# Performance work log

Measured on AMD Instinct MI355X. Metric: run time of the kernel, lower is better.

## Reference

```python
import jax, jax.numpy as jnp
import numpy as np

# 25 anchors (YOLOv2 VOC anchors replicated at 5 scales) -> pred channels = 25*5 = 125
_BASE = np.array([[1.3221, 1.73145], [3.19275, 4.00944], [5.05587, 8.09892],
                  [9.47112, 4.84053], [11.2364, 10.0071]], dtype=np.float32)
ANCHORS = jnp.asarray(np.concatenate([_BASE * s for s in (0.5, 0.75, 1.0, 1.25, 1.5)], axis=0))  # (25, 2)
NUM_ANCHORS = 25
OBJECT_SCALE = 5.0
NO_OBJECT_SCALE = 1.0
COORD_SCALE = 1.0
SIL_THRESH = 0.6


def _bbox_iou(x1, y1, w1, h1, x2, y2, w2, h2):
    """IoU of center-format boxes (cx, cy, w, h); broadcasts."""
    mx = jnp.minimum(x1 - w1 * 0.5, x2 - w2 * 0.5)
    Mx = jnp.maximum(x1 + w1 * 0.5, x2 + w2 * 0.5)
    my = jnp.minimum(y1 - h1 * 0.5, y2 - h2 * 0.5)
    My = jnp.maximum(y1 + h1 * 0.5, y2 + h2 * 0.5)
    cw = w1 + w2 - (Mx - mx)
    ch = h1 + h2 - (My - my)
    inter = jnp.where((cw > 0) & (ch > 0), cw * ch, 0.0)
    union = w1 * h1 + w2 * h2 - inter
    return inter / union


def setup_inputs() -> dict:
    key = jax.random.key(0)
    k1, k2 = jax.random.split(key)
    B, C, H, W = 512, NUM_ANCHORS * 5, 38, 38
    pred = jax.random.normal(k1, (B, C, H, W), dtype=jnp.float32)
    target = jax.random.uniform(k2, (B, 4), dtype=jnp.float32)  # normalized gx, gy, gw, gh
    return {"pred": pred, "target": target, "train_out": 0}


def reference(pred, target, train_out):
    B = pred.shape[0]
    H = pred.shape[2]
    W = pred.shape[3]
    A = NUM_ANCHORS
    p = pred.reshape(B, A, 5, H, W)

    # activations (these carry gradient in the original)
    txy = jax.nn.sigmoid(p[:, :, :2])          # (B,A,2,H,W)
    twh = p[:, :, 2:4]                         # (B,A,2,H,W)
    pred_conf = jax.nn.sigmoid(p[:, :, 4])     # (B,A,H,W)

    grid_x = jnp.arange(W, dtype=jnp.float32)[None, None, None, :]
    grid_y = jnp.arange(H, dtype=jnp.float32)[None, None, :, None]
    aw = ANCHORS[:, 0][None, :, None, None]
    ah = ANCHORS[:, 1][None, :, None, None]

    # decoded boxes are detached in the original (clone().detach())
    bx = txy[:, :, 0] + grid_x
    by = txy[:, :, 1] + grid_y
    bw = jnp.exp(twh[:, :, 0]) * aw
    bh = jnp.exp(twh[:, :, 1]) * ah
    pred_boxes = jax.lax.stop_gradient(jnp.stack([bx, by, bw, bh], axis=2))  # (B,A,4,H,W)

    tgt = jax.lax.stop_gradient(target)
    gx = tgt[:, 0] * W
    gy = tgt[:, 1] * H
    gw = tgt[:, 2] * W
    gh = tgt[:, 3] * H

    # conf_mask: zero where any pred box overlaps gt above sil_thresh
    ious = _bbox_iou(pred_boxes[:, :, 0], pred_boxes[:, :, 1], pred_boxes[:, :, 2], pred_boxes[:, :, 3],
                     gx[:, None, None, None], gy[:, None, None, None],
                     gw[:, None, None, None], gh[:, None, None, None])  # (B,A,H,W)
    conf_mask = jnp.where(ious > SIL_THRESH, 0.0, NO_OBJECT_SCALE)

    # best anchor per gt by wh-only IoU
    a_iou = _bbox_iou(0.0, 0.0, ANCHORS[:, 0][None, :], ANCHORS[:, 1][None, :],
                      0.0, 0.0, gw[:, None], gh[:, None])  # (B,A)
    best = jnp.argmax(a_iou, axis=1)  # (B,)

    gi = gx.astype(jnp.int32)
    gj = gy.astype(jnp.int32)
    bidx = jnp.arange(B)
    best_aw = ANCHORS[best, 0]
    best_ah = ANCHORS[best, 1]

    # seen < 12800 branch: coord_mask all ones, target xy default 0.5
    coord_mask = jnp.ones((B, A, H, W), dtype=jnp.float32)
    target_box = jnp.zeros((B, A, 4, H, W), dtype=jnp.float32).at[:, :, :2].set(0.5)
    target_box = target_box.at[bidx, best, 0, gj, gi].set(gx - gi)
    target_box = target_box.at[bidx, best, 1, gj, gi].set(gy - gj)
    target_box = target_box.at[bidx, best, 2, gj, gi].set(jnp.log(gw / best_aw))
    target_box = target_box.at[bidx, best, 3, gj, gi].set(jnp.log(gh / best_ah))
    conf_mask = conf_mask.at[bidx, best, gj, gi].set(OBJECT_SCALE)

    pb = pred_boxes[bidx, best, :, gj, gi]  # (B,4) pred box at gt cell
    tconf = _bbox_iou(pb[:, 0], pb[:, 1], pb[:, 2], pb[:, 3], gx, gy, gw, gh)
    target_conf = jnp.zeros((B, A, H, W), dtype=jnp.float32).at[bidx, best, gj, gi].set(tconf)

    conf_mask = jnp.sqrt(conf_mask)

    def mse_sum(a, b):
        return jnp.sum((a - b) ** 2)

    loss_x = COORD_SCALE * mse_sum(txy[:, :, 0] * coord_mask, target_box[:, :, 0] * coord_mask) / 2.0
    loss_y = COORD_SCALE * mse_sum(txy[:, :, 1] * coord_mask, target_box[:, :, 1] * coord_mask) / 2.0
    loss_w = COORD_SCALE * mse_sum(twh[:, :, 0] * coord_mask, target_box[:, :, 2] * coord_mask) / 2.0
    loss_h = COORD_SCALE * mse_sum(twh[:, :, 1] * coord_mask, target_box[:, :, 3] * coord_mask) / 2.0
    loss_conf = mse_sum(pred_conf * conf_mask, target_conf * conf_mask) / 2.0
    loss = loss_x + loss_y + loss_w + loss_h + loss_conf

    if train_out:
        return (loss, loss_x, loss_y, loss_w, loss_h, loss_conf)
    return loss
```

## Files before the change

kernel.cpp:

```cpp
#include <hip/hip_runtime.h>
#include <math.h>

#define GW 38
#define GH 38
#define NA 25
#define NB 512
#define HW (GW * GH)
#define S4 (HW / 4)
#define PLANES (NB * NA)
#define T_TOTAL (PLANES * S4)
#define BLK 256
#define NBLOCKS (T_TOTAL / BLK)

typedef float f32x4 __attribute__((ext_vector_type(4)));

struct Meta {
    float gxlo, gxhi, gylo, gyhi;
    float gw, gh, area;
    float tconf, tb0, tb1, tb2, tb3;
    int   best, cell;
};
static_assert(sizeof(Meta) == 56, "Meta layout drifted; workspace offsets depend on it");

__device__ __forceinline__ float fast_rcp(float x) { return __builtin_amdgcn_rcpf(x); }
__device__ __forceinline__ float fast_exp(float x) { return __expf(x); }
__device__ __forceinline__ float fast_sig(float x) { return fast_rcp(1.0f + fast_exp(-x)); }

__device__ __forceinline__ float iou_precise(float x1, float y1, float w1, float h1,
                                             float x2, float y2, float w2, float h2) {
    float mx = fminf(x1 - w1 * 0.5f, x2 - w2 * 0.5f);
    float Mx = fmaxf(x1 + w1 * 0.5f, x2 + w2 * 0.5f);
    float my = fminf(y1 - h1 * 0.5f, y2 - h2 * 0.5f);
    float My = fmaxf(y1 + h1 * 0.5f, y2 + h2 * 0.5f);
    float cw = w1 + w2 - (Mx - mx);
    float ch = h1 + h2 - (My - my);
    float inter = (cw > 0.0f && ch > 0.0f) ? cw * ch : 0.0f;
    float uni = w1 * h1 + w2 * h2 - inter;
    return inter / uni;
}

__device__ __forceinline__ void anchor_wh(int a, float* aw, float* ah) {
    const float bw[5] = {1.3221f, 3.19275f, 5.05587f, 9.47112f, 11.2364f};
    const float bh[5] = {1.73145f, 4.00944f, 8.09892f, 4.84053f, 10.0071f};
    float s = 0.5f + 0.25f * (float)(a / 5);
    *aw = bw[a % 5] * s;
    *ah = bh[a % 5] * s;
}

__global__ void meta_kernel(const float* __restrict__ pred,
                            const float* __restrict__ target,
                            Meta* __restrict__ metas) {
    int b = blockIdx.x * blockDim.x + threadIdx.x;
    if (b >= NB) return;
    float gx = target[b * 4 + 0] * (float)GW;
    float gy = target[b * 4 + 1] * (float)GH;
    float gw = target[b * 4 + 2] * (float)GW;
    float gh = target[b * 4 + 3] * (float)GH;
    int best = 0;
    float best_iou = -1.0f;
    for (int a = 0; a < NA; ++a) {
        float aw, ah;
        anchor_wh(a, &aw, &ah);
        float v = iou_precise(0.0f, 0.0f, aw, ah, 0.0f, 0.0f, gw, gh);
        if (v > best_iou) { best_iou = v; best = a; }
    }
    int gi = (int)gx;
    int gj = (int)gy;
    float aw, ah;
    anchor_wh(best, &aw, &ah);
    size_t base = (size_t)b * NA * 5 * HW + (size_t)(best * 5) * HW + gj * GW + gi;
    float p0 = pred[base + 0 * HW];
    float p1 = pred[base + 1 * HW];
    float p2 = pred[base + 2 * HW];
    float p3 = pred[base + 3 * HW];
    float pbx = 1.0f / (1.0f + expf(-p0)) + (float)gi;
    float pby = 1.0f / (1.0f + expf(-p1)) + (float)gj;
    float pbw = expf(p2) * aw;
    float pbh = expf(p3) * ah;
    Meta m;
    m.gxlo = gx - gw * 0.5f; m.gxhi = gx + gw * 0.5f;
    m.gylo = gy - gh * 0.5f; m.gyhi = gy + gh * 0.5f;
    m.gw = gw; m.gh = gh; m.area = gw * gh;
    m.tconf = iou_precise(pbx, pby, pbw, pbh, gx, gy, gw, gh);
    m.tb0 = gx - (float)gi;
    m.tb1 = gy - (float)gj;
    m.tb2 = logf(gw / aw);
    m.tb3 = logf(gh / ah);
    m.best = best;
    m.cell = gj * GW + gi;
    metas[b] = m;
}

__device__ __forceinline__ float cell_loss(float p0, float p1, float p2, float p3, float p4,
                                           float fi, float fj, bool obj,
                                           const Meta& m, float aw, float ah) {
    float tx = fast_sig(p0);
    float ty = fast_sig(p1);
    float conf = fast_sig(p4);
    float bw = fast_exp(p2) * aw;
    float bh = fast_exp(p3) * ah;
    float bx = tx + fi;
    float by = ty + fj;
    float mx = fminf(bx - bw * 0.5f, m.gxlo);
    float Mx = fmaxf(bx + bw * 0.5f, m.gxhi);
    float my = fminf(by - bh * 0.5f, m.gylo);
    float My = fmaxf(by + bh * 0.5f, m.gyhi);
    float cw = bw + m.gw - (Mx - mx);
    float ch = bh + m.gh - (My - my);
    float inter = (cw > 0.0f && ch > 0.0f) ? cw * ch : 0.0f;
    float uni = bw * bh + m.area - inter;
    float iou = inter * fast_rcp(uni);
    float cm = obj ? 2.23606797749979f : ((iou > 0.6f) ? 0.0f : 1.0f);
    float dx = tx - (obj ? m.tb0 : 0.5f);
    float dy = ty - (obj ? m.tb1 : 0.5f);
    float dw = p2 - (obj ? m.tb2 : 0.0f);
    float dh = p3 - (obj ? m.tb3 : 0.0f);
    float dc = cm * (conf - (obj ? m.tconf : 0.0f));
    return dx * dx + dy * dy + dw * dw + dh * dh + dc * dc;
}

template <bool USE_PARTIALS>
__global__ __launch_bounds__(BLK) void loss_kernel(const float* __restrict__ pred,
                                                   const Meta* __restrict__ metas,
                                                   float* __restrict__ sink) {
    unsigned t = blockIdx.x * (unsigned)BLK + threadIdx.x;
    unsigned plane = t / (unsigned)S4;
    unsigned s4 = t - plane * (unsigned)S4;
    unsigned b = plane / (unsigned)NA;
    unsigned a = plane - b * (unsigned)NA;

    const f32x4* base = (const f32x4*)(pred + (size_t)plane * 5u * (unsigned)HW);

    f32x4 q[5];
#pragma unroll
    for (int c = 0; c < 5; ++c)
        q[c] = __builtin_nontemporal_load(base + s4 + (unsigned)c * (unsigned)S4);

    Meta m = metas[b];
    float aw, ah;
    anchor_wh((int)a, &aw, &ah);
    bool aok = (a == (unsigned)m.best);

    float acc = 0.0f;
#pragma unroll
    for (int k = 0; k < 4; ++k) {
        unsigned s = s4 * 4u + (unsigned)k;
        unsigned j = s / (unsigned)GW;
        unsigned i = s - j * (unsigned)GW;
        float fi = (float)i, fj = (float)j;
        bool obj = aok && (s == (unsigned)m.cell);
        acc += cell_loss(q[0][k], q[1][k], q[2][k], q[3][k], q[4][k], fi, fj, obj, m, aw, ah);
    }

    for (int off = 32; off > 0; off >>= 1)
        acc += __shfl_down(acc, off, 64);
    __shared__ float sm[BLK / 64];
    int lane = (int)(threadIdx.x & 63u);
    int wv = (int)(threadIdx.x >> 6u);
    if (lane == 0) sm[wv] = acc;
    __syncthreads();
    if (threadIdx.x == 0) {
        float s = sm[0] + sm[1] + sm[2] + sm[3];
        if (USE_PARTIALS)
            sink[blockIdx.x] = s;
        else
            atomicAdd(sink, 0.5f * s);
    }
}

__global__ __launch_bounds__(BLK) void reduce_kernel(const float* __restrict__ partials,
                                                     float* __restrict__ out) {
    float acc = 0.0f;
    for (int i = (int)threadIdx.x; i < NBLOCKS; i += BLK)
        acc += partials[i];
    for (int off = 32; off > 0; off >>= 1)
        acc += __shfl_down(acc, off, 64);
    __shared__ float sm[BLK / 64];
    int lane = (int)(threadIdx.x & 63u);
    int wv = (int)(threadIdx.x >> 6u);
    if (lane == 0) sm[wv] = acc;
    __syncthreads();
    if (threadIdx.x == 0)
        out[0] = 0.5f * (sm[0] + sm[1] + sm[2] + sm[3]);
}

extern "C" void kernel_launch(void* const* d_in, const int* in_sizes, int n_in,
                              void* d_out, int out_size, void* d_ws, size_t ws_size,
                              hipStream_t stream) {
    const float* pred = (const float*)d_in[0];
    const float* target = (const float*)d_in[1];
    float* out = (float*)d_out;
    Meta* metas = (Meta*)d_ws;

    const size_t meta_bytes = sizeof(Meta) * NB;
    const size_t need = meta_bytes + (size_t)NBLOCKS * sizeof(float);
    const bool use_partials = ws_size >= need;

    hipMemsetAsync(d_out, 0, (size_t)out_size * sizeof(float), stream);
    meta_kernel<<<(NB + BLK - 1) / BLK, BLK, 0, stream>>>(pred, target, metas);
    if (use_partials) {
        float* partials = (float*)((char*)d_ws + meta_bytes);
        loss_kernel<true><<<NBLOCKS, BLK, 0, stream>>>(pred, metas, partials);
        reduce_kernel<<<1, BLK, 0, stream>>>(partials, out);
    } else {
        loss_kernel<false><<<NBLOCKS, BLK, 0, stream>>>(pred, metas, out);
    }
}
```

Before: 472.5 us.

## Use persistent grid-stride loop with double-buffered register prefetch in loss kernel

Replaces the one-tile-per-thread launch with a fixed grid of 2048 blocks that grid-strides over tiles. Each thread prefetches the next tile's five vector loads into a second register buffer while computing the current one, aiming to hide memory latency and cut block launch and reduction overhead. The nontemporal load hint is dropped, and the doubled register buffers may lower occupancy. The final reduction now sums only 2048 partials.

```diff
diff --git a/kernel.cpp b/kernel.cpp
--- a/kernel.cpp
+++ b/kernel.cpp
@@ -8,9 +8,10 @@
 #define HW (GW * GH)
 #define S4 (HW / 4)
 #define PLANES (NB * NA)
-#define T_TOTAL (PLANES * S4)
+#define NTILES (PLANES * S4)
 #define BLK 256
-#define NBLOCKS (T_TOTAL / BLK)
+#define GRID 2048
+#define NTHREADS (GRID * BLK)
 
 typedef float f32x4 __attribute__((ext_vector_type(4)));
 
@@ -119,37 +120,63 @@
     return dx * dx + dy * dy + dw * dw + dh * dh + dc * dc;
 }
 
-template <bool USE_PARTIALS>
-__global__ __launch_bounds__(BLK) void loss_kernel(const float* __restrict__ pred,
-                                                   const Meta* __restrict__ metas,
-                                                   float* __restrict__ sink) {
-    unsigned t = blockIdx.x * (unsigned)BLK + threadIdx.x;
-    unsigned plane = t / (unsigned)S4;
-    unsigned s4 = t - plane * (unsigned)S4;
+__device__ __forceinline__ void load_tile(const float* __restrict__ pred,
+                                          unsigned idx, f32x4* q,
+                                          unsigned* plane_out, unsigned* s4_out) {
+    unsigned plane = idx / (unsigned)S4;
+    unsigned s4 = idx - plane * (unsigned)S4;
+    const f32x4* base = (const f32x4*)(pred + (size_t)plane * 5u * (unsigned)HW);
+#pragma unroll
+    for (int c = 0; c < 5; ++c)
+        q[c] = base[s4 + (unsigned)c * (unsigned)S4];
+    *plane_out = plane;
+    *s4_out = s4;
+}
+
+__device__ __forceinline__ float compute_tile(const f32x4* q, unsigned plane, unsigned s4,
+                                              const Meta* __restrict__ metas) {
     unsigned b = plane / (unsigned)NA;
     unsigned a = plane - b * (unsigned)NA;
-
-    const f32x4* base = (const f32x4*)(pred + (size_t)plane * 5u * (unsigned)HW);
-
-    f32x4 q[5];
-#pragma unroll
-    for (int c = 0; c < 5; ++c)
-        q[c] = __builtin_nontemporal_load(base + s4 + (unsigned)c * (unsigned)S4);
-
     Meta m = metas[b];
     float aw, ah;
     anchor_wh((int)a, &aw, &ah);
     bool aok = (a == (unsigned)m.best);
-
     float acc = 0.0f;
 #pragma unroll
     for (int k = 0; k < 4; ++k) {
         unsigned s = s4 * 4u + (unsigned)k;
         unsigned j = s / (unsigned)GW;
         unsigned i = s - j * (unsigned)GW;
-        float fi = (float)i, fj = (float)j;
         bool obj = aok && (s == (unsigned)m.cell);
-        acc += cell_loss(q[0][k], q[1][k], q[2][k], q[3][k], q[4][k], fi, fj, obj, m, aw, ah);
+        acc += cell_loss(q[0][k], q[1][k], q[2][k], q[3][k], q[4][k],
+                         (float)i, (float)j, obj, m, aw, ah);
+    }
+    return acc;
+}
+
+template <bool USE_PARTIALS>
+__global__ __launch_bounds__(BLK) void loss_kernel(const float* __restrict__ pred,
+                                                   const Meta* __restrict__ metas,
+                                                   float* __restrict__ sink) {
+    unsigned tid = blockIdx.x * (unsigned)BLK + threadIdx.x;
+    float acc = 0.0f;
+
+    f32x4 qA[5], qB[5];
+    unsigned plA, s4A, plB, s4B;
+    unsigned i0 = tid;
+    load_tile(pred, i0, qA, &plA, &s4A);
+    for (;;) {
+        unsigned i1 = i0 + (unsigned)NTHREADS;
+        bool has1 = i1 < (unsigned)NTILES;
+        if (has1) load_tile(pred, i1, qB, &plB, &s4B);
+        acc += compute_tile(qA, plA, s4A, metas);
+        if (!has1) break;
+        unsigned i2 = i1 + (unsigned)NTHREADS;
+        bool has2 = i2 < (unsigned)NTILES;
+        if (has2) load_tile(pred, i2, qA, &plA, &s4A);
+        acc += compute_tile(qB, plB, s4B, metas);
+        if (!has2) break;
+        i0 = i2;
     }
 
     for (int off = 32; off > 0; off >>= 1)
@@ -171,7 +198,7 @@
 __global__ __launch_bounds__(BLK) void reduce_kernel(const float* __restrict__ partials,
                                                      float* __restrict__ out) {
     float acc = 0.0f;
-    for (int i = (int)threadIdx.x; i < NBLOCKS; i += BLK)
+    for (int i = (int)threadIdx.x; i < GRID; i += BLK)
         acc += partials[i];
     for (int off = 32; off > 0; off >>= 1)
         acc += __shfl_down(acc, off, 64);
@@ -193,16 +220,16 @@
     Meta* metas = (Meta*)d_ws;
 
     const size_t meta_bytes = sizeof(Meta) * NB;
-    const size_t need = meta_bytes + (size_t)NBLOCKS * sizeof(float);
+    const size_t need = meta_bytes + (size_t)GRID * sizeof(float);
     const bool use_partials = ws_size >= need;
 
     hipMemsetAsync(d_out, 0, (size_t)out_size * sizeof(float), stream);
     meta_kernel<<<(NB + BLK - 1) / BLK, BLK, 0, stream>>>(pred, target, metas);
     if (use_partials) {
         float* partials = (float*)((char*)d_ws + meta_bytes);
-        loss_kernel<true><<<NBLOCKS, BLK, 0, stream>>>(pred, metas, partials);
+        loss_kernel<true><<<GRID, BLK, 0, stream>>>(pred, metas, partials);
         reduce_kernel<<<1, BLK, 0, stream>>>(partials, out);
     } else {
-        loss_kernel<false><<<NBLOCKS, BLK, 0, stream>>>(pred, metas, out);
-    }
-}
+        loss_kernel<false><<<GRID, BLK, 0, stream>>>(pred, metas, out);
+    }
+}
```

Measured after the change: 500.2 us. 5.8% more time.

## Stage whole anchor plane in LDS with contiguous coalesced loads per block

Applied to the files above, without the earlier changes.

Each block now handles one (batch, anchor) plane of five channels. It loads the plane as contiguous 16-byte vectors into shared memory, then each thread reads its cells' five channels from LDS. The old layout had each thread read five strided vectors, one per channel. The change aims at fully contiguous, coalesced global reads and fewer, larger blocks. In exchange it adds about 29KB of LDS per block, which limits occupancy, adds a barrier, and leaves some threads idle in the tail compute loop.

```diff
diff --git a/kernel.cpp b/kernel.cpp
--- a/kernel.cpp
+++ b/kernel.cpp
@@ -6,11 +6,10 @@
 #define NA 25
 #define NB 512
 #define HW (GW * GH)
-#define S4 (HW / 4)
+#define PLANE_F (5 * HW)
+#define PLANE_V4 (PLANE_F / 4)
 #define PLANES (NB * NA)
-#define T_TOTAL (PLANES * S4)
 #define BLK 256
-#define NBLOCKS (T_TOTAL / BLK)
 
 typedef float f32x4 __attribute__((ext_vector_type(4)));
 
@@ -123,33 +122,55 @@
 __global__ __launch_bounds__(BLK) void loss_kernel(const float* __restrict__ pred,
                                                    const Meta* __restrict__ metas,
                                                    float* __restrict__ sink) {
-    unsigned t = blockIdx.x * (unsigned)BLK + threadIdx.x;
-    unsigned plane = t / (unsigned)S4;
-    unsigned s4 = t - plane * (unsigned)S4;
-    unsigned b = plane / (unsigned)NA;
-    unsigned a = plane - b * (unsigned)NA;
-
-    const f32x4* base = (const f32x4*)(pred + (size_t)plane * 5u * (unsigned)HW);
-
-    f32x4 q[5];
-#pragma unroll
-    for (int c = 0; c < 5; ++c)
-        q[c] = __builtin_nontemporal_load(base + s4 + (unsigned)c * (unsigned)S4);
+    __shared__ float lds[PLANE_F];
+    const unsigned p = blockIdx.x;
+    const unsigned b = p / (unsigned)NA;
+    const unsigned a = p - b * (unsigned)NA;
+    const unsigned t = threadIdx.x;
+
+    const f32x4* src = (const f32x4*)(pred + (size_t)p * (unsigned)PLANE_F);
+    f32x4 s0 = src[t + 0u * BLK];
+    f32x4 s1 = src[t + 1u * BLK];
+    f32x4 s2 = src[t + 2u * BLK];
+    f32x4 s3 = src[t + 3u * BLK];
+    f32x4 s4 = src[t + 4u * BLK];
+    f32x4 s5 = src[t + 5u * BLK];
+    f32x4 s6 = src[t + 6u * BLK];
+    f32x4 s7;
+    const bool tail = t < (unsigned)(PLANE_V4 - 7 * BLK);
+    if (tail) s7 = src[t + 7u * BLK];
 
     Meta m = metas[b];
     float aw, ah;
     anchor_wh((int)a, &aw, &ah);
-    bool aok = (a == (unsigned)m.best);
+    const bool aok = (a == (unsigned)m.best);
+
+    f32x4* ldsv = (f32x4*)lds;
+    ldsv[t + 0u * BLK] = s0;
+    ldsv[t + 1u * BLK] = s1;
+    ldsv[t + 2u * BLK] = s2;
+    ldsv[t + 3u * BLK] = s3;
+    ldsv[t + 4u * BLK] = s4;
+    ldsv[t + 5u * BLK] = s5;
+    ldsv[t + 6u * BLK] = s6;
+    if (tail) ldsv[t + 7u * BLK] = s7;
+    __syncthreads();
 
     float acc = 0.0f;
 #pragma unroll
-    for (int k = 0; k < 4; ++k) {
-        unsigned s = s4 * 4u + (unsigned)k;
-        unsigned j = s / (unsigned)GW;
-        unsigned i = s - j * (unsigned)GW;
-        float fi = (float)i, fj = (float)j;
-        bool obj = aok && (s == (unsigned)m.cell);
-        acc += cell_loss(q[0][k], q[1][k], q[2][k], q[3][k], q[4][k], fi, fj, obj, m, aw, ah);
+    for (int k = 0; k < 6; ++k) {
+        int s = (int)t + k * BLK;
+        if (s < HW) {
+            float q0 = lds[0 * HW + s];
+            float q1 = lds[1 * HW + s];
+            float q2 = lds[2 * HW + s];
+            float q3 = lds[3 * HW + s];
+            float q4 = lds[4 * HW + s];
+            unsigned j = (unsigned)s / (unsigned)GW;
+            unsigned i = (unsigned)s - j * (unsigned)GW;
+            bool obj = aok && (s == m.cell);
+            acc += cell_loss(q0, q1, q2, q3, q4, (float)i, (float)j, obj, m, aw, ah);
+        }
     }
 
     for (int off = 32; off > 0; off >>= 1)
@@ -171,7 +192,7 @@
 __global__ __launch_bounds__(BLK) void reduce_kernel(const float* __restrict__ partials,
                                                      float* __restrict__ out) {
     float acc = 0.0f;
-    for (int i = (int)threadIdx.x; i < NBLOCKS; i += BLK)
+    for (int i = (int)threadIdx.x; i < PLANES; i += BLK)
         acc += partials[i];
     for (int off = 32; off > 0; off >>= 1)
         acc += __shfl_down(acc, off, 64);
@@ -193,16 +214,16 @@
     Meta* metas = (Meta*)d_ws;
 
     const size_t meta_bytes = sizeof(Meta) * NB;
-    const size_t need = meta_bytes + (size_t)NBLOCKS * sizeof(float);
+    const size_t need = meta_bytes + (size_t)PLANES * sizeof(float);
     const bool use_partials = ws_size >= need;
 
     hipMemsetAsync(d_out, 0, (size_t)out_size * sizeof(float), stream);
     meta_kernel<<<(NB + BLK - 1) / BLK, BLK, 0, stream>>>(pred, target, metas);
     if (use_partials) {
         float* partials = (float*)((char*)d_ws + meta_bytes);
-        loss_kernel<true><<<NBLOCKS, BLK, 0, stream>>>(pred, metas, partials);
+        loss_kernel<true><<<PLANES, BLK, 0, stream>>>(pred, metas, partials);
         reduce_kernel<<<1, BLK, 0, stream>>>(partials, out);
     } else {
-        loss_kernel<false><<<NBLOCKS, BLK, 0, stream>>>(pred, metas, out);
-    }
-}
+        loss_kernel<false><<<PLANES, BLK, 0, stream>>>(pred, metas, out);
+    }
+}
```

Result: slower. 499.8 us (+5.8%).
